# Performance work log

Hardware: AMD Instinct MI355X
Metric: run time of the kernel (lower is better)

The kernel has to match this reference:

```python
import jax, jax.numpy as jnp
import numpy as np

B, S, H, E, V = 64, 256, 1024, 256, 32000

def setup_inputs() -> dict:
    key = jax.random.key(0)
    ks = jax.random.split(key, 16)
    sc = 0.02
    return {
        'x': jax.random.randint(ks[0], (B, 1), 0, V),
        'dec_hs': jax.random.normal(ks[1], (1, B, H), jnp.float32),
        'enc_output': jax.random.normal(ks[2], (S, B, H), jnp.float32),
        'emb_table': jax.random.normal(ks[3], (V, E), jnp.float32) * sc,
        'w1_W': jax.random.normal(ks[4], (H, H), jnp.float32) * sc,
        'w1_b': jnp.zeros((H,), jnp.float32),
        'w2_W': jax.random.normal(ks[5], (H, H), jnp.float32) * sc,
        'w2_b': jnp.zeros((H,), jnp.float32),
        'v_W': jax.random.normal(ks[6], (1, H), jnp.float32) * sc,
        'v_b': jnp.zeros((1,), jnp.float32),
        'gru_W_ih': jax.random.normal(ks[7], (3 * H, H + E), jnp.float32) * sc,
        'gru_W_hh': jax.random.normal(ks[8], (3 * H, H), jnp.float32) * sc,
        'gru_b_ih': jnp.zeros((3 * H,), jnp.float32),
        'gru_b_hh': jnp.zeros((3 * H,), jnp.float32),
        'fc_W': jax.random.normal(ks[9], (V, H), jnp.float32) * sc,
        'fc_b': jnp.zeros((V,), jnp.float32),
    }

def reference(x, dec_hs, enc_output, emb_table, w1_W, w1_b, w2_W, w2_b,
              v_W, v_b, gru_W_ih, gru_W_hh, gru_b_ih, gru_b_hh, fc_W, fc_b):
    # ---- Bahdanau additive attention ----
    dec = jnp.transpose(dec_hs, (1, 0, 2))        # [B,1,H]
    enc = jnp.transpose(enc_output, (1, 0, 2))    # [B,S,H]
    feat = jnp.tanh(dec @ w1_W.T + w1_b + enc @ w2_W.T + w2_b)  # [B,S,H]
    scores = feat @ v_W.T + v_b                   # [B,S,1]
    attn = jax.nn.softmax(scores, axis=1)         # [B,S,1]
    context = jnp.sum(attn * enc, axis=1)         # [B,H]
    # ---- embedding lookup + concat ----
    emb = emb_table[x[:, 0]]                      # [B,E]
    gru_in = jnp.concatenate([context, emb], axis=-1)  # [B,H+E]
    # ---- single-step GRU (PyTorch gate convention) ----
    h = dec_hs[0]                                 # [B,H]
    gi = gru_in @ gru_W_ih.T + gru_b_ih           # [B,3H]
    gh = h @ gru_W_hh.T + gru_b_hh                # [B,3H]
    gi_r, gi_z, gi_n = jnp.split(gi, 3, axis=-1)
    gh_r, gh_z, gh_n = jnp.split(gh, 3, axis=-1)
    r = jax.nn.sigmoid(gi_r + gh_r)
    z = jax.nn.sigmoid(gi_z + gh_z)
    n = jnp.tanh(gi_n + r * gh_n)
    h_new = (1.0 - z) * n + z * h                 # [B,H]
    # ---- output projection ----
    fc_out = h_new @ fc_W.T + fc_b                # [B,V]
    return fc_out, h_new[None], attn
```

## Files before the change

### kernel.cpp

```cpp
#include <hip/hip_runtime.h>

#define BB 64
#define SS 256
#define HH 1024
#define EE 256
#define VV 32000

typedef unsigned short u16;
typedef __attribute__((ext_vector_type(4))) unsigned short u16x4;
typedef __attribute__((ext_vector_type(8))) short s16x8;
typedef __attribute__((ext_vector_type(4))) float f32x4;

typedef const void __attribute__((address_space(1)))* gas_p;
typedef void __attribute__((address_space(3)))* las_p;

__device__ __forceinline__ u16 f2bf(float f) {
  unsigned u = __builtin_bit_cast(unsigned, f);
  u += 0x7fffu + ((u >> 16) & 1u);
  return (u16)(u >> 16);
}
__device__ __forceinline__ float bf2f(u16 u) {
  return __builtin_bit_cast(float, ((unsigned)u) << 16);
}
__device__ __forceinline__ void gload16(const void* g, void* l) {
  __builtin_amdgcn_global_load_lds((gas_p)g, (las_p)l, 16, 0, 0);
}
#define MFMA16(a, b, c) __builtin_amdgcn_mfma_f32_16x16x32_bf16(a, b, c, 0, 0, 0)

__global__ __launch_bounds__(256) void k_convert(const float* __restrict__ enc,
    const float* __restrict__ w2, const float* __restrict__ dec,
    u16* __restrict__ Ap, u16* __restrict__ w2b, u16* __restrict__ hb) {
  int bid = blockIdx.x, t = threadIdx.x;
  const float* src;
  u16* dst;
  if (bid < BB * SS) {
    int b = bid >> 8, s = bid & 255;
    src = enc + (size_t)(s * BB + b) * HH;
    dst = Ap + (size_t)bid * HH;
  } else if (bid < BB * SS + HH) {
    int r = bid - BB * SS;
    src = w2 + (size_t)r * HH;
    dst = w2b + (size_t)r * HH;
  } else {
    int b = bid - (BB * SS + HH);
    src = dec + (size_t)b * HH;
    dst = hb + (size_t)b * HH;
  }
  f32x4 v = *(const f32x4*)(src + t * 4);
  u16x4 o = { f2bf(v[0]), f2bf(v[1]), f2bf(v[2]), f2bf(v[3]) };
  *(u16x4*)(dst + t * 4) = o;
}

__global__ __launch_bounds__(256) void k_dbmm(const u16* __restrict__ hb,
    const float* __restrict__ w1, float* __restrict__ dbp) {
  int kc = blockIdx.y;
  int kb = kc * 128;
  int n0 = blockIdx.x * 128;
  __shared__ u16 Ws[2][128 * 32];
  int t = threadIdx.x, lane = t & 63, w = t >> 6;
  int wm = w >> 1, wn = w & 1, l15 = lane & 15, lg = lane >> 4;
  f32x4 acc[2][4] = {};
  int kx = (lg ^ ((l15 >> 1) & 3)) * 8;
  int wrow = t >> 1, wh = t & 1;
  int xr = (wrow >> 1) & 3;
  int s0 = (2 * wh) ^ xr, s1 = (2 * wh + 1) ^ xr;
  const float* gW = w1 + (size_t)(n0 + wrow) * HH + kb + wh * 16;
  const u16* gA = hb + kb + lg * 8;
  f32x4 c0 = *(const f32x4*)(gW);
  f32x4 c1 = *(const f32x4*)(gW + 4);
  f32x4 c2 = *(const f32x4*)(gW + 8);
  f32x4 c3 = *(const f32x4*)(gW + 12);
  s16x8 a0 = *(const s16x8*)(gA + (size_t)(wm * 32 + l15) * HH);
  s16x8 a1 = *(const s16x8*)(gA + (size_t)(wm * 32 + 16 + l15) * HH);
  {
    u16* lw = &Ws[0][wrow * 32];
    u16x4 o0 = { f2bf(c0[0]), f2bf(c0[1]), f2bf(c0[2]), f2bf(c0[3]) };
    u16x4 o1 = { f2bf(c1[0]), f2bf(c1[1]), f2bf(c1[2]), f2bf(c1[3]) };
    u16x4 o2 = { f2bf(c2[0]), f2bf(c2[1]), f2bf(c2[2]), f2bf(c2[3]) };
    u16x4 o3 = { f2bf(c3[0]), f2bf(c3[1]), f2bf(c3[2]), f2bf(c3[3]) };
    *(u16x4*)(lw + s0 * 8) = o0; *(u16x4*)(lw + s0 * 8 + 4) = o1;
    *(u16x4*)(lw + s1 * 8) = o2; *(u16x4*)(lw + s1 * 8 + 4) = o3;
  }
  __syncthreads();
  for (int it = 0; it < 4; ++it) {
    int nlast = (it < 3);
    f32x4 n0v, n1v, n2v, n3v;
    s16x8 an0, an1;
    if (nlast) {
      int k1 = (it + 1) * 32;
      n0v = *(const f32x4*)(gW + k1);
      n1v = *(const f32x4*)(gW + k1 + 4);
      n2v = *(const f32x4*)(gW + k1 + 8);
      n3v = *(const f32x4*)(gW + k1 + 12);
      an0 = *(const s16x8*)(gA + (size_t)(wm * 32 + l15) * HH + k1);
      an1 = *(const s16x8*)(gA + (size_t)(wm * 32 + 16 + l15) * HH + k1);
    }
    const u16* wb = Ws[it & 1];
    s16x8 bfr[4];
#pragma unroll
    for (int ni = 0; ni < 4; ++ni)
      bfr[ni] = *(const s16x8*)&wb[(wn * 64 + ni * 16 + l15) * 32 + kx];
#pragma unroll
    for (int ni = 0; ni < 4; ++ni) {
      acc[0][ni] = MFMA16(a0, bfr[ni], acc[0][ni]);
      acc[1][ni] = MFMA16(a1, bfr[ni], acc[1][ni]);
    }
    if (nlast) {
      u16* lw = &Ws[(it + 1) & 1][wrow * 32];
      u16x4 o0 = { f2bf(n0v[0]), f2bf(n0v[1]), f2bf(n0v[2]), f2bf(n0v[3]) };
      u16x4 o1 = { f2bf(n1v[0]), f2bf(n1v[1]), f2bf(n1v[2]), f2bf(n1v[3]) };
      u16x4 o2 = { f2bf(n2v[0]), f2bf(n2v[1]), f2bf(n2v[2]), f2bf(n2v[3]) };
      u16x4 o3 = { f2bf(n3v[0]), f2bf(n3v[1]), f2bf(n3v[2]), f2bf(n3v[3]) };
      *(u16x4*)(lw + s0 * 8) = o0; *(u16x4*)(lw + s0 * 8 + 4) = o1;
      *(u16x4*)(lw + s1 * 8) = o2; *(u16x4*)(lw + s1 * 8 + 4) = o3;
      a0 = an0; a1 = an1;
    }
    __syncthreads();
  }
  float* Pb = dbp + (size_t)kc * 64 * HH;
#pragma unroll
  for (int mi = 0; mi < 2; ++mi)
#pragma unroll
    for (int ni = 0; ni < 4; ++ni)
#pragma unroll
      for (int r = 0; r < 4; ++r) {
        int m = wm * 32 + mi * 16 + lg * 4 + r;
        int n = n0 + wn * 64 + ni * 16 + l15;
        Pb[(size_t)m * HH + n] = acc[mi][ni][r];
      }
}

__global__ __launch_bounds__(256) void k_biggemm(const u16* __restrict__ Ap,
    const u16* __restrict__ Bw, const float* __restrict__ w1b,
    const float* __restrict__ w2bias, const float* __restrict__ dbp,
    const float* __restrict__ vW, float* __restrict__ sp) {
  __shared__ u16 As[128 * 64];
  __shared__ u16 Bs[128 * 64];
  __shared__ float sc[2][128];
  int bid = blockIdx.x;
  int mt = ((bid >> 6) << 3) | (bid & 7);
  int nt = (bid >> 3) & 7;
  int t = threadIdx.x, lane = t & 63, w = t >> 6;
  int wm = w >> 1, wn = w & 1, l15 = lane & 15, lg = lane >> 4;
  int m0 = mt * 128, n0 = nt * 128;
  int b = m0 >> 8;
  f32x4 acc[4][4] = {};
  int srow = w * 32 + (lane >> 3);
  int cswz = ((lane & 7) ^ (lane >> 3)) * 8;
  const u16* gA = Ap + (size_t)(m0 + srow) * HH + cswz;
  const u16* gB = Bw + (size_t)(n0 + srow) * HH + cswz;
  u16* lA = As + w * 32 * 64;
  u16* lB = Bs + w * 32 * 64;
  for (int it = 0; it < 16; ++it) {
    int k0 = it * 64;
#pragma unroll
    for (int i = 0; i < 4; ++i)
      gload16(gA + (size_t)i * 8 * HH + k0, lA + i * 8 * 64);
#pragma unroll
    for (int i = 0; i < 4; ++i)
      gload16(gB + (size_t)i * 8 * HH + k0, lB + i * 8 * 64);
    __syncthreads();
#pragma unroll
    for (int kk = 0; kk < 2; ++kk) {
      s16x8 af[4], bfr[4];
#pragma unroll
      for (int mi = 0; mi < 4; ++mi) {
        int row = wm * 64 + mi * 16 + l15;
        int slot = (kk * 4 + lg) ^ (row & 7);
        af[mi] = *(const s16x8*)&As[row * 64 + slot * 8];
      }
#pragma unroll
      for (int ni = 0; ni < 4; ++ni) {
        int row = wn * 64 + ni * 16 + l15;
        int slot = (kk * 4 + lg) ^ (row & 7);
        bfr[ni] = *(const s16x8*)&Bs[row * 64 + slot * 8];
      }
#pragma unroll
      for (int mi = 0; mi < 4; ++mi)
#pragma unroll
        for (int ni = 0; ni < 4; ++ni)
          acc[mi][ni] = MFMA16(af[mi], bfr[ni], acc[mi][ni]);
    }
    __syncthreads();
  }
  const float* vv = vW + n0;
  float dbs[4];
#pragma unroll
  for (int ni = 0; ni < 4; ++ni) {
    int nl = wn * 64 + ni * 16 + l15;
    int n = n0 + nl;
    float s = w1b[n] + w2bias[n];
#pragma unroll
    for (int p = 0; p < 8; ++p) s += dbp[(size_t)p * 64 * HH + (size_t)b * HH + n];
    dbs[ni] = s;
  }
#pragma unroll
  for (int mi = 0; mi < 4; ++mi) {
#pragma unroll
    for (int r = 0; r < 4; ++r) {
      float p = 0.f;
#pragma unroll
      for (int ni = 0; ni < 4; ++ni) {
        int nl = wn * 64 + ni * 16 + l15;
        p += tanhf(acc[mi][ni][r] + dbs[ni]) * vv[nl];
      }
      p += __shfl_xor(p, 1); p += __shfl_xor(p, 2);
      p += __shfl_xor(p, 4); p += __shfl_xor(p, 8);
      if (l15 == 0) sc[wn][wm * 64 + mi * 16 + lg * 4 + r] = p;
    }
  }
  __syncthreads();
  if (t < 128) sp[(size_t)(m0 + t) * 8 + nt] = sc[0][t] + sc[1][t];
}

__global__ __launch_bounds__(256) void k_ctxsm(const float* __restrict__ sp,
    const float* __restrict__ vb, const u16* __restrict__ Ap,
    float* __restrict__ attn, float* __restrict__ ctxp) {
  int sc = blockIdx.x, b = blockIdx.y, t = threadIdx.x;
  int lane = t & 63, w = t >> 6;
  const float* row = sp + (size_t)(b * SS + t) * 8;
  f32x4 a = *(const f32x4*)row;
  f32x4 c = *(const f32x4*)(row + 4);
  float score = a[0] + a[1] + a[2] + a[3] + c[0] + c[1] + c[2] + c[3] + vb[0];
  __shared__ float rmax[4], rsum[4], at[SS];
  float m = score;
  for (int mk = 1; mk < 64; mk <<= 1) m = fmaxf(m, __shfl_xor(m, mk));
  if (lane == 0) rmax[w] = m;
  __syncthreads();
  m = fmaxf(fmaxf(rmax[0], rmax[1]), fmaxf(rmax[2], rmax[3]));
  float e = expf(score - m);
  float ssum = e;
  for (int mk = 1; mk < 64; mk <<= 1) ssum += __shfl_xor(ssum, mk);
  if (lane == 0) rsum[w] = ssum;
  __syncthreads();
  float tot = rsum[0] + rsum[1] + rsum[2] + rsum[3];
  float av = e / tot;
  at[t] = av;
  if (sc == 0) attn[(size_t)b * SS + t] = av;
  __syncthreads();
  const u16* base = Ap + (size_t)(b * SS + sc * 32) * HH + t * 4;
  float a0 = 0.f, a1 = 0.f, a2 = 0.f, a3 = 0.f;
#pragma unroll 4
  for (int s = 0; s < 32; ++s) {
    u16x4 v = *(const u16x4*)(base + (size_t)s * HH);
    float w_ = at[sc * 32 + s];
    a0 += w_ * bf2f(v[0]); a1 += w_ * bf2f(v[1]);
    a2 += w_ * bf2f(v[2]); a3 += w_ * bf2f(v[3]);
  }
  f32x4 o = { a0, a1, a2, a3 };
  *(f32x4*)&ctxp[(size_t)(b * 8 + sc) * HH + t * 4] = o;
}

__global__ __launch_bounds__(256) void k_ctxcomb(const float* __restrict__ ctxp,
    const int* __restrict__ x, const float* __restrict__ emb,
    u16* __restrict__ gin) {
  int b = blockIdx.x, t = threadIdx.x;
  f32x4 s = {0.f, 0.f, 0.f, 0.f};
#pragma unroll
  for (int p = 0; p < 8; ++p)
    s += *(const f32x4*)&ctxp[(size_t)(b * 8 + p) * HH + t * 4];
  u16x4 o = { f2bf(s[0]), f2bf(s[1]), f2bf(s[2]), f2bf(s[3]) };
  *(u16x4*)(gin + (size_t)b * 1280 + t * 4) = o;
  int xb = x[b];
  gin[(size_t)b * 1280 + HH + t] = f2bf(emb[(size_t)xb * EE + t]);
}

__global__ __launch_bounds__(256) void k_gru(const u16* __restrict__ gin,
    const u16* __restrict__ hb, const float* __restrict__ Wih,
    const float* __restrict__ Whh, float* __restrict__ P) {
  int y = blockIdx.y;
  int z = (y >= 5);
  const u16* Ab = z ? hb : gin;
  const float* Wf = z ? Whh : Wih;
  int K = z ? HH : (HH + EE);
  int kb = (z ? (y - 5) : y) * 256;
  int n0 = blockIdx.x * 128;
  __shared__ u16 Ws[2][128 * 32];
  int t = threadIdx.x, lane = t & 63, w = t >> 6;
  int wm = w >> 1, wn = w & 1, l15 = lane & 15, lg = lane >> 4;
  f32x4 acc[2][4] = {};
  int kx = (lg ^ ((l15 >> 1) & 3)) * 8;
  int wrow = t >> 1, wh = t & 1;
  int xr = (wrow >> 1) & 3;
  int s0 = (2 * wh) ^ xr, s1 = (2 * wh + 1) ^ xr;
  const float* gW = Wf + (size_t)(n0 + wrow) * K + kb + wh * 16;
  const u16* gA = Ab + kb + lg * 8;
  f32x4 c0 = *(const f32x4*)(gW);
  f32x4 c1 = *(const f32x4*)(gW + 4);
  f32x4 c2 = *(const f32x4*)(gW + 8);
  f32x4 c3 = *(const f32x4*)(gW + 12);
  s16x8 a0 = *(const s16x8*)(gA + (size_t)(wm * 32 + l15) * K);
  s16x8 a1 = *(const s16x8*)(gA + (size_t)(wm * 32 + 16 + l15) * K);
  {
    u16* lw = &Ws[0][wrow * 32];
    u16x4 o0 = { f2bf(c0[0]), f2bf(c0[1]), f2bf(c0[2]), f2bf(c0[3]) };
    u16x4 o1 = { f2bf(c1[0]), f2bf(c1[1]), f2bf(c1[2]), f2bf(c1[3]) };
    u16x4 o2 = { f2bf(c2[0]), f2bf(c2[1]), f2bf(c2[2]), f2bf(c2[3]) };
    u16x4 o3 = { f2bf(c3[0]), f2bf(c3[1]), f2bf(c3[2]), f2bf(c3[3]) };
    *(u16x4*)(lw + s0 * 8) = o0; *(u16x4*)(lw + s0 * 8 + 4) = o1;
    *(u16x4*)(lw + s1 * 8) = o2; *(u16x4*)(lw + s1 * 8 + 4) = o3;
  }
  __syncthreads();
  for (int it = 0; it < 8; ++it) {
    int nlast = (it < 7);
    f32x4 n0v, n1v, n2v, n3v;
    s16x8 an0, an1;
    if (nlast) {
      int k1 = (it + 1) * 32;
      n0v = *(const f32x4*)(gW + k1);
      n1v = *(const f32x4*)(gW + k1 + 4);
      n2v = *(const f32x4*)(gW + k1 + 8);
      n3v = *(const f32x4*)(gW + k1 + 12);
      an0 = *(const s16x8*)(gA + (size_t)(wm * 32 + l15) * K + k1);
      an1 = *(const s16x8*)(gA + (size_t)(wm * 32 + 16 + l15) * K + k1);
    }
    const u16* wb = Ws[it & 1];
    s16x8 bfr[4];
#pragma unroll
    for (int ni = 0; ni < 4; ++ni)
      bfr[ni] = *(const s16x8*)&wb[(wn * 64 + ni * 16 + l15) * 32 + kx];
#pragma unroll
    for (int ni = 0; ni < 4; ++ni) {
      acc[0][ni] = MFMA16(a0, bfr[ni], acc[0][ni]);
      acc[1][ni] = MFMA16(a1, bfr[ni], acc[1][ni]);
    }
    if (nlast) {
      u16* lw = &Ws[(it + 1) & 1][wrow * 32];
      u16x4 o0 = { f2bf(n0v[0]), f2bf(n0v[1]), f2bf(n0v[2]), f2bf(n0v[3]) };
      u16x4 o1 = { f2bf(n1v[0]), f2bf(n1v[1]), f2bf(n1v[2]), f2bf(n1v[3]) };
      u16x4 o2 = { f2bf(n2v[0]), f2bf(n2v[1]), f2bf(n2v[2]), f2bf(n2v[3]) };
      u16x4 o3 = { f2bf(n3v[0]), f2bf(n3v[1]), f2bf(n3v[2]), f2bf(n3v[3]) };
      *(u16x4*)(lw + s0 * 8) = o0; *(u16x4*)(lw + s0 * 8 + 4) = o1;
      *(u16x4*)(lw + s1 * 8) = o2; *(u16x4*)(lw + s1 * 8 + 4) = o3;
      a0 = an0; a1 = an1;
    }
    __syncthreads();
  }
  float* Pb = P + (size_t)y * 64 * 3072;
#pragma unroll
  for (int mi = 0; mi < 2; ++mi)
#pragma unroll
    for (int ni = 0; ni < 4; ++ni)
#pragma unroll
      for (int r = 0; r < 4; ++r) {
        int m = wm * 32 + mi * 16 + lg * 4 + r;
        int n = n0 + wn * 64 + ni * 16 + l15;
        Pb[(size_t)m * 3072 + n] = acc[mi][ni][r];
      }
}

__global__ __launch_bounds__(256) void k_gates(const float* __restrict__ P,
    const float* __restrict__ bih, const float* __restrict__ bhh,
    const float* __restrict__ dec, float* __restrict__ hn_out,
    u16* __restrict__ hnb) {
  int b = blockIdx.x, t = threadIdx.x;
#pragma unroll
  for (int j = 0; j < 4; ++j) {
    int h = t + j * 256;
    float gir = 0.f, giz = 0.f, gin_ = 0.f, ghr = 0.f, ghz = 0.f, ghn = 0.f;
#pragma unroll
    for (int y = 0; y < 5; ++y) {
      const float* r = P + (size_t)(y * 64 + b) * 3072;
      gir += r[h]; giz += r[h + 1024]; gin_ += r[h + 2048];
    }
#pragma unroll
    for (int y = 0; y < 4; ++y) {
      const float* r = P + (size_t)((5 + y) * 64 + b) * 3072;
      ghr += r[h]; ghz += r[h + 1024]; ghn += r[h + 2048];
    }
    float rr = 1.f / (1.f + expf(-(gir + bih[h] + ghr + bhh[h])));
    float zz = 1.f / (1.f + expf(-(giz + bih[1024 + h] + ghz + bhh[1024 + h])));
    float nn = tanhf(gin_ + bih[2048 + h] + rr * (ghn + bhh[2048 + h]));
    float hv = dec[(size_t)b * HH + h];
    float hnew = (1.f - zz) * nn + zz * hv;
    hn_out[(size_t)b * HH + h] = hnew;
    hnb[(size_t)b * HH + h] = f2bf(hnew);
  }
}

__global__ __launch_bounds__(256) void k_fc(const u16* __restrict__ hnb,
    const float* __restrict__ W, const float* __restrict__ bias,
    float* __restrict__ out) {
  int n0 = blockIdx.x * 64;
  __shared__ u16 Ws[2][64 * 32];
  int t = threadIdx.x, lane = t & 63, w = t >> 6;
  int wm = w >> 1, wn = w & 1, l15 = lane & 15, lg = lane >> 4;
  f32x4 acc[2][2] = {};
  int kx = (lg ^ ((l15 >> 1) & 3)) * 8;
  int wrow = t >> 2;
  int sq = ((t & 3) ^ ((t >> 3) & 3)) * 8;
  const float* gW = W + (size_t)(n0 + wrow) * HH + (t & 3) * 8;
  const u16* gA = hnb + lg * 8;
  f32x4 c0 = *(const f32x4*)(gW);
  f32x4 c1 = *(const f32x4*)(gW + 4);
  s16x8 a0 = *(const s16x8*)(gA + (size_t)(wm * 32 + l15) * HH);
  s16x8 a1 = *(const s16x8*)(gA + (size_t)(wm * 32 + 16 + l15) * HH);
  {
    u16* lw = &Ws[0][wrow * 32 + sq];
    u16x4 o0 = { f2bf(c0[0]), f2bf(c0[1]), f2bf(c0[2]), f2bf(c0[3]) };
    u16x4 o1 = { f2bf(c1[0]), f2bf(c1[1]), f2bf(c1[2]), f2bf(c1[3]) };
    *(u16x4*)(lw) = o0; *(u16x4*)(lw + 4) = o1;
  }
  __syncthreads();
  for (int it = 0; it < 32; ++it) {
    int nlast = (it < 31);
    f32x4 n0v, n1v;
    s16x8 an0, an1;
    if (nlast) {
      int k1 = (it + 1) * 32;
      n0v = *(const f32x4*)(gW + k1);
      n1v = *(const f32x4*)(gW + k1 + 4);
      an0 = *(const s16x8*)(gA + (size_t)(wm * 32 + l15) * HH + k1);
      an1 = *(const s16x8*)(gA + (size_t)(wm * 32 + 16 + l15) * HH + k1);
    }
    const u16* wb = Ws[it & 1];
    s16x8 bfr[2];
#pragma unroll
    for (int ni = 0; ni < 2; ++ni)
      bfr[ni] = *(const s16x8*)&wb[(wn * 32 + ni * 16 + l15) * 32 + kx];
#pragma unroll
    for (int ni = 0; ni < 2; ++ni) {
      acc[0][ni] = MFMA16(a0, bfr[ni], acc[0][ni]);
      acc[1][ni] = MFMA16(a1, bfr[ni], acc[1][ni]);
    }
    if (nlast) {
      u16* lw = &Ws[(it + 1) & 1][wrow * 32 + sq];
      u16x4 o0 = { f2bf(n0v[0]), f2bf(n0v[1]), f2bf(n0v[2]), f2bf(n0v[3]) };
      u16x4 o1 = { f2bf(n1v[0]), f2bf(n1v[1]), f2bf(n1v[2]), f2bf(n1v[3]) };
      *(u16x4*)(lw) = o0; *(u16x4*)(lw + 4) = o1;
      a0 = an0; a1 = an1;
    }
    __syncthreads();
  }
#pragma unroll
  for (int mi = 0; mi < 2; ++mi)
#pragma unroll
    for (int ni = 0; ni < 2; ++ni)
#pragma unroll
      for (int r = 0; r < 4; ++r) {
        int m = wm * 32 + mi * 16 + lg * 4 + r;
        int n = n0 + wn * 32 + ni * 16 + l15;
        out[(size_t)m * VV + n] = acc[mi][ni][r] + bias[n];
      }
}

extern "C" void kernel_launch(void* const* d_in, const int* in_sizes, int n_in,
                              void* d_out, int out_size, void* d_ws, size_t ws_size,
                              hipStream_t stream) {
  const int*   x      = (const int*)   d_in[0];
  const float* dec    = (const float*) d_in[1];
  const float* enc    = (const float*) d_in[2];
  const float* emb    = (const float*) d_in[3];
  const float* w1     = (const float*) d_in[4];
  const float* w1b    = (const float*) d_in[5];
  const float* w2     = (const float*) d_in[6];
  const float* w2bias = (const float*) d_in[7];
  const float* vW     = (const float*) d_in[8];
  const float* vb     = (const float*) d_in[9];
  const float* Wih    = (const float*) d_in[10];
  const float* Whh    = (const float*) d_in[11];
  const float* bih    = (const float*) d_in[12];
  const float* bhh    = (const float*) d_in[13];
  const float* fcW    = (const float*) d_in[14];
  const float* fcb    = (const float*) d_in[15];
  float* out = (float*)d_out;
  char* ws = (char*)d_ws;
  u16*   Ap    = (u16*)(ws);
  u16*   w2b   = (u16*)(ws + 33554432);
  u16*   hb    = (u16*)(ws + 35651584);
  u16*   gin   = (u16*)(ws + 35782656);
  u16*   hnb   = (u16*)(ws + 35946496);
  float* sp    = (float*)(ws + 36339712);
  float* P     = (float*)(ws + 36864000);
  float* dbp   = P;
  float* ctxp  = P + 524288;
  float* hn   = out + 2048000;
  float* attn = out + 2113536;

  k_convert<<<BB * SS + HH + BB, 256, 0, stream>>>(enc, w2, dec, Ap, w2b, hb);
  k_dbmm<<<dim3(8, 8), 256, 0, stream>>>(hb, w1, dbp);
  k_biggemm<<<1024, 256, 0, stream>>>(Ap, w2b, w1b, w2bias, dbp, vW, sp);
  k_ctxsm<<<dim3(8, BB), 256, 0, stream>>>(sp, vb, Ap, attn, ctxp);
  k_ctxcomb<<<BB, 256, 0, stream>>>(ctxp, x, emb, gin);
  k_gru<<<dim3(24, 9), 256, 0, stream>>>(gin, hb, Wih, Whh, P);
  k_gates<<<BB, 256, 0, stream>>>(P, bih, bhh, dec, hn, hnb);
  k_fc<<<500, 256, 0, stream>>>(hnb, fcW, fcb, out);
}
```

Before: 145.9 us.

## Fuse convert with decoder matmul, switch big GEMM to 32x32 MFMA, widen gates grid

Merges the fp32-to-bf16 conversion kernel and the decoder-state projection into one launch: extra blocks compute the projection by converting dec directly instead of reading the bf16 copy. The attention GEMM uses 32x32x16 MFMA tiles instead of 16x16x32, which needs fewer LDS fragment loads per MFMA, and the epilogue reduction is adjusted to match. The gate kernel spreads each batch row over four blocks for more parallelism. Together these cut one launch and reduce LDS traffic, at the cost of more register pressure in the GEMM accumulators.

```diff
diff --git a/kernel.cpp b/kernel.cpp
--- a/kernel.cpp
+++ b/kernel.cpp
@@ -10,6 +10,7 @@
 typedef __attribute__((ext_vector_type(4))) unsigned short u16x4;
 typedef __attribute__((ext_vector_type(8))) short s16x8;
 typedef __attribute__((ext_vector_type(4))) float f32x4;
+typedef __attribute__((ext_vector_type(16))) float f32x16;
 
 typedef const void __attribute__((address_space(1)))* gas_p;
 typedef void __attribute__((address_space(3)))* las_p;
@@ -22,42 +23,54 @@
 __device__ __forceinline__ float bf2f(u16 u) {
   return __builtin_bit_cast(float, ((unsigned)u) << 16);
 }
+__device__ __forceinline__ s16x8 cvt8(f32x4 a, f32x4 b) {
+  s16x8 r;
+  r[0] = (short)f2bf(a[0]); r[1] = (short)f2bf(a[1]);
+  r[2] = (short)f2bf(a[2]); r[3] = (short)f2bf(a[3]);
+  r[4] = (short)f2bf(b[0]); r[5] = (short)f2bf(b[1]);
+  r[6] = (short)f2bf(b[2]); r[7] = (short)f2bf(b[3]);
+  return r;
+}
 __device__ __forceinline__ void gload16(const void* g, void* l) {
   __builtin_amdgcn_global_load_lds((gas_p)g, (las_p)l, 16, 0, 0);
 }
 #define MFMA16(a, b, c) __builtin_amdgcn_mfma_f32_16x16x32_bf16(a, b, c, 0, 0, 0)
-
-__global__ __launch_bounds__(256) void k_convert(const float* __restrict__ enc,
+#define MFMA32(a, b, c) __builtin_amdgcn_mfma_f32_32x32x16_bf16(a, b, c, 0, 0, 0)
+
+#define NCONV (BB * SS + HH + BB)
+__global__ __launch_bounds__(256) void k_convdb(const float* __restrict__ enc,
     const float* __restrict__ w2, const float* __restrict__ dec,
-    u16* __restrict__ Ap, u16* __restrict__ w2b, u16* __restrict__ hb) {
+    const float* __restrict__ w1,
+    u16* __restrict__ Ap, u16* __restrict__ w2b, u16* __restrict__ hb,
+    float* __restrict__ dbp) {
+  __shared__ u16 Ws[2][128 * 32];
   int bid = blockIdx.x, t = threadIdx.x;
-  const float* src;
-  u16* dst;
-  if (bid < BB * SS) {
-    int b = bid >> 8, s = bid & 255;
-    src = enc + (size_t)(s * BB + b) * HH;
-    dst = Ap + (size_t)bid * HH;
-  } else if (bid < BB * SS + HH) {
-    int r = bid - BB * SS;
-    src = w2 + (size_t)r * HH;
-    dst = w2b + (size_t)r * HH;
-  } else {
-    int b = bid - (BB * SS + HH);
-    src = dec + (size_t)b * HH;
-    dst = hb + (size_t)b * HH;
-  }
-  f32x4 v = *(const f32x4*)(src + t * 4);
-  u16x4 o = { f2bf(v[0]), f2bf(v[1]), f2bf(v[2]), f2bf(v[3]) };
-  *(u16x4*)(dst + t * 4) = o;
-}
-
-__global__ __launch_bounds__(256) void k_dbmm(const u16* __restrict__ hb,
-    const float* __restrict__ w1, float* __restrict__ dbp) {
-  int kc = blockIdx.y;
+  if (bid < NCONV) {
+    const float* src;
+    u16* dst;
+    if (bid < BB * SS) {
+      int b = bid >> 8, s = bid & 255;
+      src = enc + (size_t)(s * BB + b) * HH;
+      dst = Ap + (size_t)bid * HH;
+    } else if (bid < BB * SS + HH) {
+      int r = bid - BB * SS;
+      src = w2 + (size_t)r * HH;
+      dst = w2b + (size_t)r * HH;
+    } else {
+      int b = bid - (BB * SS + HH);
+      src = dec + (size_t)b * HH;
+      dst = hb + (size_t)b * HH;
+    }
+    f32x4 v = *(const f32x4*)(src + t * 4);
+    u16x4 o = { f2bf(v[0]), f2bf(v[1]), f2bf(v[2]), f2bf(v[3]) };
+    *(u16x4*)(dst + t * 4) = o;
+    return;
+  }
+  int bid2 = bid - NCONV;
+  int nt = bid2 & 7, kc = bid2 >> 3;
   int kb = kc * 128;
-  int n0 = blockIdx.x * 128;
-  __shared__ u16 Ws[2][128 * 32];
-  int t = threadIdx.x, lane = t & 63, w = t >> 6;
+  int n0 = nt * 128;
+  int lane = t & 63, w = t >> 6;
   int wm = w >> 1, wn = w & 1, l15 = lane & 15, lg = lane >> 4;
   f32x4 acc[2][4] = {};
   int kx = (lg ^ ((l15 >> 1) & 3)) * 8;
@@ -65,13 +78,15 @@
   int xr = (wrow >> 1) & 3;
   int s0 = (2 * wh) ^ xr, s1 = (2 * wh + 1) ^ xr;
   const float* gW = w1 + (size_t)(n0 + wrow) * HH + kb + wh * 16;
-  const u16* gA = hb + kb + lg * 8;
+  const float* dA = dec + kb + lg * 8;
   f32x4 c0 = *(const f32x4*)(gW);
   f32x4 c1 = *(const f32x4*)(gW + 4);
   f32x4 c2 = *(const f32x4*)(gW + 8);
   f32x4 c3 = *(const f32x4*)(gW + 12);
-  s16x8 a0 = *(const s16x8*)(gA + (size_t)(wm * 32 + l15) * HH);
-  s16x8 a1 = *(const s16x8*)(gA + (size_t)(wm * 32 + 16 + l15) * HH);
+  const float* r0 = dA + (size_t)(wm * 32 + l15) * HH;
+  const float* r1 = dA + (size_t)(wm * 32 + 16 + l15) * HH;
+  s16x8 a0 = cvt8(*(const f32x4*)r0, *(const f32x4*)(r0 + 4));
+  s16x8 a1 = cvt8(*(const f32x4*)r1, *(const f32x4*)(r1 + 4));
   {
     u16* lw = &Ws[0][wrow * 32];
     u16x4 o0 = { f2bf(c0[0]), f2bf(c0[1]), f2bf(c0[2]), f2bf(c0[3]) };
@@ -92,8 +107,8 @@
       n1v = *(const f32x4*)(gW + k1 + 4);
       n2v = *(const f32x4*)(gW + k1 + 8);
       n3v = *(const f32x4*)(gW + k1 + 12);
-      an0 = *(const s16x8*)(gA + (size_t)(wm * 32 + l15) * HH + k1);
-      an1 = *(const s16x8*)(gA + (size_t)(wm * 32 + 16 + l15) * HH + k1);
+      an0 = cvt8(*(const f32x4*)(r0 + k1), *(const f32x4*)(r0 + k1 + 4));
+      an1 = cvt8(*(const f32x4*)(r1 + k1), *(const f32x4*)(r1 + k1 + 4));
     }
     const u16* wb = Ws[it & 1];
     s16x8 bfr[4];
@@ -141,10 +156,11 @@
   int mt = ((bid >> 6) << 3) | (bid & 7);
   int nt = (bid >> 3) & 7;
   int t = threadIdx.x, lane = t & 63, w = t >> 6;
-  int wm = w >> 1, wn = w & 1, l15 = lane & 15, lg = lane >> 4;
+  int wm = w >> 1, wn = w & 1;
+  int l31 = lane & 31, lh = lane >> 5;
   int m0 = mt * 128, n0 = nt * 128;
   int b = m0 >> 8;
-  f32x4 acc[4][4] = {};
+  f32x16 acc[2][2] = {};
   int srow = w * 32 + (lane >> 3);
   int cswz = ((lane & 7) ^ (lane >> 3)) * 8;
   const u16* gA = Ap + (size_t)(m0 + srow) * HH + cswz;
@@ -161,52 +177,50 @@
       gload16(gB + (size_t)i * 8 * HH + k0, lB + i * 8 * 64);
     __syncthreads();
 #pragma unroll
-    for (int kk = 0; kk < 2; ++kk) {
-      s16x8 af[4], bfr[4];
-#pragma unroll
-      for (int mi = 0; mi < 4; ++mi) {
-        int row = wm * 64 + mi * 16 + l15;
-        int slot = (kk * 4 + lg) ^ (row & 7);
+    for (int kc = 0; kc < 4; ++kc) {
+      s16x8 af[2], bfr[2];
+#pragma unroll
+      for (int mi = 0; mi < 2; ++mi) {
+        int row = wm * 64 + mi * 32 + l31;
+        int slot = (kc * 2 + lh) ^ (row & 7);
         af[mi] = *(const s16x8*)&As[row * 64 + slot * 8];
       }
 #pragma unroll
-      for (int ni = 0; ni < 4; ++ni) {
-        int row = wn * 64 + ni * 16 + l15;
-        int slot = (kk * 4 + lg) ^ (row & 7);
+      for (int ni = 0; ni < 2; ++ni) {
+        int row = wn * 64 + ni * 32 + l31;
+        int slot = (kc * 2 + lh) ^ (row & 7);
         bfr[ni] = *(const s16x8*)&Bs[row * 64 + slot * 8];
       }
 #pragma unroll
-      for (int mi = 0; mi < 4; ++mi)
-#pragma unroll
-        for (int ni = 0; ni < 4; ++ni)
-          acc[mi][ni] = MFMA16(af[mi], bfr[ni], acc[mi][ni]);
+      for (int mi = 0; mi < 2; ++mi)
+#pragma unroll
+        for (int ni = 0; ni < 2; ++ni)
+          acc[mi][ni] = MFMA32(af[mi], bfr[ni], acc[mi][ni]);
     }
     __syncthreads();
   }
-  const float* vv = vW + n0;
-  float dbs[4];
-#pragma unroll
-  for (int ni = 0; ni < 4; ++ni) {
-    int nl = wn * 64 + ni * 16 + l15;
-    int n = n0 + nl;
+  float dbs[2], vvv[2];
+#pragma unroll
+  for (int ni = 0; ni < 2; ++ni) {
+    int n = n0 + wn * 64 + ni * 32 + l31;
     float s = w1b[n] + w2bias[n];
 #pragma unroll
-    for (int p = 0; p < 8; ++p) s += dbp[(size_t)p * 64 * HH + (size_t)b * HH + n];
+    for (int p = 0; p < 8; ++p)
+      s += dbp[(size_t)p * 64 * HH + (size_t)b * HH + n];
     dbs[ni] = s;
-  }
-#pragma unroll
-  for (int mi = 0; mi < 4; ++mi) {
-#pragma unroll
-    for (int r = 0; r < 4; ++r) {
-      float p = 0.f;
-#pragma unroll
-      for (int ni = 0; ni < 4; ++ni) {
-        int nl = wn * 64 + ni * 16 + l15;
-        p += tanhf(acc[mi][ni][r] + dbs[ni]) * vv[nl];
-      }
+    vvv[ni] = vW[n];
+  }
+#pragma unroll
+  for (int mi = 0; mi < 2; ++mi) {
+#pragma unroll
+    for (int r = 0; r < 16; ++r) {
+      float p = tanhf(acc[mi][0][r] + dbs[0]) * vvv[0]
+              + tanhf(acc[mi][1][r] + dbs[1]) * vvv[1];
       p += __shfl_xor(p, 1); p += __shfl_xor(p, 2);
       p += __shfl_xor(p, 4); p += __shfl_xor(p, 8);
-      if (l15 == 0) sc[wn][wm * 64 + mi * 16 + lg * 4 + r] = p;
+      p += __shfl_xor(p, 16);
+      if (l31 == 0)
+        sc[wn][wm * 64 + mi * 32 + (r & 3) + 8 * (r >> 2) + 4 * lh] = p;
     }
   }
   __syncthreads();
@@ -353,29 +367,26 @@
     const float* __restrict__ bih, const float* __restrict__ bhh,
     const float* __restrict__ dec, float* __restrict__ hn_out,
     u16* __restrict__ hnb) {
-  int b = blockIdx.x, t = threadIdx.x;
-#pragma unroll
-  for (int j = 0; j < 4; ++j) {
-    int h = t + j * 256;
-    float gir = 0.f, giz = 0.f, gin_ = 0.f, ghr = 0.f, ghz = 0.f, ghn = 0.f;
-#pragma unroll
-    for (int y = 0; y < 5; ++y) {
-      const float* r = P + (size_t)(y * 64 + b) * 3072;
-      gir += r[h]; giz += r[h + 1024]; gin_ += r[h + 2048];
-    }
-#pragma unroll
-    for (int y = 0; y < 4; ++y) {
-      const float* r = P + (size_t)((5 + y) * 64 + b) * 3072;
-      ghr += r[h]; ghz += r[h + 1024]; ghn += r[h + 2048];
-    }
-    float rr = 1.f / (1.f + expf(-(gir + bih[h] + ghr + bhh[h])));
-    float zz = 1.f / (1.f + expf(-(giz + bih[1024 + h] + ghz + bhh[1024 + h])));
-    float nn = tanhf(gin_ + bih[2048 + h] + rr * (ghn + bhh[2048 + h]));
-    float hv = dec[(size_t)b * HH + h];
-    float hnew = (1.f - zz) * nn + zz * hv;
-    hn_out[(size_t)b * HH + h] = hnew;
-    hnb[(size_t)b * HH + h] = f2bf(hnew);
-  }
+  int b = blockIdx.y, t = threadIdx.x;
+  int h = blockIdx.x * 256 + t;
+  float gir = 0.f, giz = 0.f, gin_ = 0.f, ghr = 0.f, ghz = 0.f, ghn = 0.f;
+#pragma unroll
+  for (int y = 0; y < 5; ++y) {
+    const float* r = P + (size_t)(y * 64 + b) * 3072;
+    gir += r[h]; giz += r[h + 1024]; gin_ += r[h + 2048];
+  }
+#pragma unroll
+  for (int y = 0; y < 4; ++y) {
+    const float* r = P + (size_t)((5 + y) * 64 + b) * 3072;
+    ghr += r[h]; ghz += r[h + 1024]; ghn += r[h + 2048];
+  }
+  float rr = 1.f / (1.f + expf(-(gir + bih[h] + ghr + bhh[h])));
+  float zz = 1.f / (1.f + expf(-(giz + bih[1024 + h] + ghz + bhh[1024 + h])));
+  float nn = tanhf(gin_ + bih[2048 + h] + rr * (ghn + bhh[2048 + h]));
+  float hv = dec[(size_t)b * HH + h];
+  float hnew = (1.f - zz) * nn + zz * hv;
+  hn_out[(size_t)b * HH + h] = hnew;
+  hnb[(size_t)b * HH + h] = f2bf(hnew);
 }
 
 __global__ __launch_bounds__(256) void k_fc(const u16* __restrict__ hnb,
@@ -477,12 +488,11 @@
   float* hn   = out + 2048000;
   float* attn = out + 2113536;
 
-  k_convert<<<BB * SS + HH + BB, 256, 0, stream>>>(enc, w2, dec, Ap, w2b, hb);
-  k_dbmm<<<dim3(8, 8), 256, 0, stream>>>(hb, w1, dbp);
+  k_convdb<<<NCONV + 64, 256, 0, stream>>>(enc, w2, dec, w1, Ap, w2b, hb, dbp);
   k_biggemm<<<1024, 256, 0, stream>>>(Ap, w2b, w1b, w2bias, dbp, vW, sp);
   k_ctxsm<<<dim3(8, BB), 256, 0, stream>>>(sp, vb, Ap, attn, ctxp);
   k_ctxcomb<<<BB, 256, 0, stream>>>(ctxp, x, emb, gin);
   k_gru<<<dim3(24, 9), 256, 0, stream>>>(gin, hb, Wih, Whh, P);
-  k_gates<<<BB, 256, 0, stream>>>(P, bih, bhh, dec, hn, hnb);
+  k_gates<<<dim3(4, BB), 256, 0, stream>>>(P, bih, bhh, dec, hn, hnb);
   k_fc<<<500, 256, 0, stream>>>(hnb, fcW, fcb, out);
 }
```

New measurement: 155.5 us. +6.6%, slower.

## Fuse dec-projection GEMM into convert kernel, widen GRU k-tile, spread gates grid

Applied to the files above, without the earlier changes.

Folds the small dec@W1 GEMM into the conversion kernel as extra blocks. Those blocks read dec in fp32 and convert it in registers, so they no longer wait on the bf16 hb buffer, and one launch is removed. The GRU GEMM k-step grows from 32 to 64, with a wider LDS tile and 8-way XOR swizzle, halving the barrier-separated iterations. The gates kernel is split over a 4x64 grid instead of 64 blocks to raise parallelism. The cost is more LDS and registers per GRU block, and a mixed-role fused kernel.

```diff
diff --git a/kernel.cpp b/kernel.cpp
--- a/kernel.cpp
+++ b/kernel.cpp
@@ -22,42 +22,53 @@
 __device__ __forceinline__ float bf2f(u16 u) {
   return __builtin_bit_cast(float, ((unsigned)u) << 16);
 }
+__device__ __forceinline__ s16x8 cvt8(f32x4 a, f32x4 b) {
+  s16x8 r;
+  r[0] = (short)f2bf(a[0]); r[1] = (short)f2bf(a[1]);
+  r[2] = (short)f2bf(a[2]); r[3] = (short)f2bf(a[3]);
+  r[4] = (short)f2bf(b[0]); r[5] = (short)f2bf(b[1]);
+  r[6] = (short)f2bf(b[2]); r[7] = (short)f2bf(b[3]);
+  return r;
+}
 __device__ __forceinline__ void gload16(const void* g, void* l) {
   __builtin_amdgcn_global_load_lds((gas_p)g, (las_p)l, 16, 0, 0);
 }
 #define MFMA16(a, b, c) __builtin_amdgcn_mfma_f32_16x16x32_bf16(a, b, c, 0, 0, 0)
 
-__global__ __launch_bounds__(256) void k_convert(const float* __restrict__ enc,
+#define NCONV (BB * SS + HH + BB)
+__global__ __launch_bounds__(256) void k_convdb(const float* __restrict__ enc,
     const float* __restrict__ w2, const float* __restrict__ dec,
-    u16* __restrict__ Ap, u16* __restrict__ w2b, u16* __restrict__ hb) {
+    const float* __restrict__ w1,
+    u16* __restrict__ Ap, u16* __restrict__ w2b, u16* __restrict__ hb,
+    float* __restrict__ dbp) {
+  __shared__ u16 Ws[2][128 * 32];
   int bid = blockIdx.x, t = threadIdx.x;
-  const float* src;
-  u16* dst;
-  if (bid < BB * SS) {
-    int b = bid >> 8, s = bid & 255;
-    src = enc + (size_t)(s * BB + b) * HH;
-    dst = Ap + (size_t)bid * HH;
-  } else if (bid < BB * SS + HH) {
-    int r = bid - BB * SS;
-    src = w2 + (size_t)r * HH;
-    dst = w2b + (size_t)r * HH;
-  } else {
-    int b = bid - (BB * SS + HH);
-    src = dec + (size_t)b * HH;
-    dst = hb + (size_t)b * HH;
-  }
-  f32x4 v = *(const f32x4*)(src + t * 4);
-  u16x4 o = { f2bf(v[0]), f2bf(v[1]), f2bf(v[2]), f2bf(v[3]) };
-  *(u16x4*)(dst + t * 4) = o;
-}
-
-__global__ __launch_bounds__(256) void k_dbmm(const u16* __restrict__ hb,
-    const float* __restrict__ w1, float* __restrict__ dbp) {
-  int kc = blockIdx.y;
+  if (bid < NCONV) {
+    const float* src;
+    u16* dst;
+    if (bid < BB * SS) {
+      int b = bid >> 8, s = bid & 255;
+      src = enc + (size_t)(s * BB + b) * HH;
+      dst = Ap + (size_t)bid * HH;
+    } else if (bid < BB * SS + HH) {
+      int r = bid - BB * SS;
+      src = w2 + (size_t)r * HH;
+      dst = w2b + (size_t)r * HH;
+    } else {
+      int b = bid - (BB * SS + HH);
+      src = dec + (size_t)b * HH;
+      dst = hb + (size_t)b * HH;
+    }
+    f32x4 v = *(const f32x4*)(src + t * 4);
+    u16x4 o = { f2bf(v[0]), f2bf(v[1]), f2bf(v[2]), f2bf(v[3]) };
+    *(u16x4*)(dst + t * 4) = o;
+    return;
+  }
+  int bid2 = bid - NCONV;
+  int nt = bid2 & 7, kc = bid2 >> 3;
   int kb = kc * 128;
-  int n0 = blockIdx.x * 128;
-  __shared__ u16 Ws[2][128 * 32];
-  int t = threadIdx.x, lane = t & 63, w = t >> 6;
+  int n0 = nt * 128;
+  int lane = t & 63, w = t >> 6;
   int wm = w >> 1, wn = w & 1, l15 = lane & 15, lg = lane >> 4;
   f32x4 acc[2][4] = {};
   int kx = (lg ^ ((l15 >> 1) & 3)) * 8;
@@ -65,13 +76,15 @@
   int xr = (wrow >> 1) & 3;
   int s0 = (2 * wh) ^ xr, s1 = (2 * wh + 1) ^ xr;
   const float* gW = w1 + (size_t)(n0 + wrow) * HH + kb + wh * 16;
-  const u16* gA = hb + kb + lg * 8;
+  const float* dA = dec + kb + lg * 8;
   f32x4 c0 = *(const f32x4*)(gW);
   f32x4 c1 = *(const f32x4*)(gW + 4);
   f32x4 c2 = *(const f32x4*)(gW + 8);
   f32x4 c3 = *(const f32x4*)(gW + 12);
-  s16x8 a0 = *(const s16x8*)(gA + (size_t)(wm * 32 + l15) * HH);
-  s16x8 a1 = *(const s16x8*)(gA + (size_t)(wm * 32 + 16 + l15) * HH);
+  const float* r0 = dA + (size_t)(wm * 32 + l15) * HH;
+  const float* r1 = dA + (size_t)(wm * 32 + 16 + l15) * HH;
+  s16x8 a0 = cvt8(*(const f32x4*)r0, *(const f32x4*)(r0 + 4));
+  s16x8 a1 = cvt8(*(const f32x4*)r1, *(const f32x4*)(r1 + 4));
   {
     u16* lw = &Ws[0][wrow * 32];
     u16x4 o0 = { f2bf(c0[0]), f2bf(c0[1]), f2bf(c0[2]), f2bf(c0[3]) };
@@ -92,8 +105,8 @@
       n1v = *(const f32x4*)(gW + k1 + 4);
       n2v = *(const f32x4*)(gW + k1 + 8);
       n3v = *(const f32x4*)(gW + k1 + 12);
-      an0 = *(const s16x8*)(gA + (size_t)(wm * 32 + l15) * HH + k1);
-      an1 = *(const s16x8*)(gA + (size_t)(wm * 32 + 16 + l15) * HH + k1);
+      an0 = cvt8(*(const f32x4*)(r0 + k1), *(const f32x4*)(r0 + k1 + 4));
+      an1 = cvt8(*(const f32x4*)(r1 + k1), *(const f32x4*)(r1 + k1 + 4));
     }
     const u16* wb = Ws[it & 1];
     s16x8 bfr[4];
@@ -275,64 +288,83 @@
   int K = z ? HH : (HH + EE);
   int kb = (z ? (y - 5) : y) * 256;
   int n0 = blockIdx.x * 128;
-  __shared__ u16 Ws[2][128 * 32];
+  __shared__ u16 Ws[2][128 * 64];
   int t = threadIdx.x, lane = t & 63, w = t >> 6;
   int wm = w >> 1, wn = w & 1, l15 = lane & 15, lg = lane >> 4;
   f32x4 acc[2][4] = {};
-  int kx = (lg ^ ((l15 >> 1) & 3)) * 8;
   int wrow = t >> 1, wh = t & 1;
-  int xr = (wrow >> 1) & 3;
-  int s0 = (2 * wh) ^ xr, s1 = (2 * wh + 1) ^ xr;
-  const float* gW = Wf + (size_t)(n0 + wrow) * K + kb + wh * 16;
+  int s_[4];
+#pragma unroll
+  for (int j = 0; j < 4; ++j) s_[j] = ((4 * wh + j) ^ (wrow & 7)) * 8;
+  const float* gW = Wf + (size_t)(n0 + wrow) * K + kb + wh * 32;
   const u16* gA = Ab + kb + lg * 8;
-  f32x4 c0 = *(const f32x4*)(gW);
-  f32x4 c1 = *(const f32x4*)(gW + 4);
-  f32x4 c2 = *(const f32x4*)(gW + 8);
-  f32x4 c3 = *(const f32x4*)(gW + 12);
-  s16x8 a0 = *(const s16x8*)(gA + (size_t)(wm * 32 + l15) * K);
-  s16x8 a1 = *(const s16x8*)(gA + (size_t)(wm * 32 + 16 + l15) * K);
+  const u16* rA0 = gA + (size_t)(wm * 32 + l15) * K;
+  const u16* rA1 = gA + (size_t)(wm * 32 + 16 + l15) * K;
+  f32x4 c0, c1, c2, c3, c4, c5, c6, c7;
+  c0 = *(const f32x4*)(gW);      c1 = *(const f32x4*)(gW + 4);
+  c2 = *(const f32x4*)(gW + 8);  c3 = *(const f32x4*)(gW + 12);
+  c4 = *(const f32x4*)(gW + 16); c5 = *(const f32x4*)(gW + 20);
+  c6 = *(const f32x4*)(gW + 24); c7 = *(const f32x4*)(gW + 28);
+  s16x8 a00 = *(const s16x8*)(rA0);
+  s16x8 a01 = *(const s16x8*)(rA0 + 32);
+  s16x8 a10 = *(const s16x8*)(rA1);
+  s16x8 a11 = *(const s16x8*)(rA1 + 32);
   {
-    u16* lw = &Ws[0][wrow * 32];
-    u16x4 o0 = { f2bf(c0[0]), f2bf(c0[1]), f2bf(c0[2]), f2bf(c0[3]) };
-    u16x4 o1 = { f2bf(c1[0]), f2bf(c1[1]), f2bf(c1[2]), f2bf(c1[3]) };
-    u16x4 o2 = { f2bf(c2[0]), f2bf(c2[1]), f2bf(c2[2]), f2bf(c2[3]) };
-    u16x4 o3 = { f2bf(c3[0]), f2bf(c3[1]), f2bf(c3[2]), f2bf(c3[3]) };
-    *(u16x4*)(lw + s0 * 8) = o0; *(u16x4*)(lw + s0 * 8 + 4) = o1;
-    *(u16x4*)(lw + s1 * 8) = o2; *(u16x4*)(lw + s1 * 8 + 4) = o3;
-  }
-  __syncthreads();
-  for (int it = 0; it < 8; ++it) {
-    int nlast = (it < 7);
-    f32x4 n0v, n1v, n2v, n3v;
-    s16x8 an0, an1;
+    u16* lw = &Ws[0][wrow * 64];
+    *(u16x4*)(lw + s_[0]) = (u16x4){ f2bf(c0[0]), f2bf(c0[1]), f2bf(c0[2]), f2bf(c0[3]) };
+    *(u16x4*)(lw + s_[0] + 4) = (u16x4){ f2bf(c1[0]), f2bf(c1[1]), f2bf(c1[2]), f2bf(c1[3]) };
+    *(u16x4*)(lw + s_[1]) = (u16x4){ f2bf(c2[0]), f2bf(c2[1]), f2bf(c2[2]), f2bf(c2[3]) };
+    *(u16x4*)(lw + s_[1] + 4) = (u16x4){ f2bf(c3[0]), f2bf(c3[1]), f2bf(c3[2]), f2bf(c3[3]) };
+    *(u16x4*)(lw + s_[2]) = (u16x4){ f2bf(c4[0]), f2bf(c4[1]), f2bf(c4[2]), f2bf(c4[3]) };
+    *(u16x4*)(lw + s_[2] + 4) = (u16x4){ f2bf(c5[0]), f2bf(c5[1]), f2bf(c5[2]), f2bf(c5[3]) };
+    *(u16x4*)(lw + s_[3]) = (u16x4){ f2bf(c6[0]), f2bf(c6[1]), f2bf(c6[2]), f2bf(c6[3]) };
+    *(u16x4*)(lw + s_[3] + 4) = (u16x4){ f2bf(c7[0]), f2bf(c7[1]), f2bf(c7[2]), f2bf(c7[3]) };
+  }
+  __syncthreads();
+  for (int it = 0; it < 4; ++it) {
+    int nlast = (it < 3);
+    f32x4 n0v, n1v, n2v, n3v, n4v, n5v, n6v, n7v;
+    s16x8 b00, b01, b10, b11;
     if (nlast) {
-      int k1 = (it + 1) * 32;
-      n0v = *(const f32x4*)(gW + k1);
-      n1v = *(const f32x4*)(gW + k1 + 4);
-      n2v = *(const f32x4*)(gW + k1 + 8);
-      n3v = *(const f32x4*)(gW + k1 + 12);
-      an0 = *(const s16x8*)(gA + (size_t)(wm * 32 + l15) * K + k1);
-      an1 = *(const s16x8*)(gA + (size_t)(wm * 32 + 16 + l15) * K + k1);
+      int k1 = (it + 1) * 64;
+      n0v = *(const f32x4*)(gW + k1);      n1v = *(const f32x4*)(gW + k1 + 4);
+      n2v = *(const f32x4*)(gW + k1 + 8);  n3v = *(const f32x4*)(gW + k1 + 12);
+      n4v = *(const f32x4*)(gW + k1 + 16); n5v = *(const f32x4*)(gW + k1 + 20);
+      n6v = *(const f32x4*)(gW + k1 + 24); n7v = *(const f32x4*)(gW + k1 + 28);
+      b00 = *(const s16x8*)(rA0 + k1);
+      b01 = *(const s16x8*)(rA0 + k1 + 32);
+      b10 = *(const s16x8*)(rA1 + k1);
+      b11 = *(const s16x8*)(rA1 + k1 + 32);
     }
     const u16* wb = Ws[it & 1];
-    s16x8 bfr[4];
-#pragma unroll
-    for (int ni = 0; ni < 4; ++ni)
-      bfr[ni] = *(const s16x8*)&wb[(wn * 64 + ni * 16 + l15) * 32 + kx];
-#pragma unroll
-    for (int ni = 0; ni < 4; ++ni) {
-      acc[0][ni] = MFMA16(a0, bfr[ni], acc[0][ni]);
-      acc[1][ni] = MFMA16(a1, bfr[ni], acc[1][ni]);
+#pragma unroll
+    for (int kk = 0; kk < 2; ++kk) {
+      s16x8 bfr[4];
+#pragma unroll
+      for (int ni = 0; ni < 4; ++ni) {
+        int row = wn * 64 + ni * 16 + l15;
+        int slot = (kk * 4 + lg) ^ (row & 7);
+        bfr[ni] = *(const s16x8*)&wb[row * 64 + slot * 8];
+      }
+      s16x8 fa0 = kk ? a01 : a00;
+      s16x8 fa1 = kk ? a11 : a10;
+#pragma unroll
+      for (int ni = 0; ni < 4; ++ni) {
+        acc[0][ni] = MFMA16(fa0, bfr[ni], acc[0][ni]);
+        acc[1][ni] = MFMA16(fa1, bfr[ni], acc[1][ni]);
+      }
     }
     if (nlast) {
-      u16* lw = &Ws[(it + 1) & 1][wrow * 32];
-      u16x4 o0 = { f2bf(n0v[0]), f2bf(n0v[1]), f2bf(n0v[2]), f2bf(n0v[3]) };
-      u16x4 o1 = { f2bf(n1v[0]), f2bf(n1v[1]), f2bf(n1v[2]), f2bf(n1v[3]) };
-      u16x4 o2 = { f2bf(n2v[0]), f2bf(n2v[1]), f2bf(n2v[2]), f2bf(n2v[3]) };
-      u16x4 o3 = { f2bf(n3v[0]), f2bf(n3v[1]), f2bf(n3v[2]), f2bf(n3v[3]) };
-      *(u16x4*)(lw + s0 * 8) = o0; *(u16x4*)(lw + s0 * 8 + 4) = o1;
-      *(u16x4*)(lw + s1 * 8) = o2; *(u16x4*)(lw + s1 * 8 + 4) = o3;
-      a0 = an0; a1 = an1;
+      u16* lw = &Ws[(it + 1) & 1][wrow * 64];
+      *(u16x4*)(lw + s_[0]) = (u16x4){ f2bf(n0v[0]), f2bf(n0v[1]), f2bf(n0v[2]), f2bf(n0v[3]) };
+      *(u16x4*)(lw + s_[0] + 4) = (u16x4){ f2bf(n1v[0]), f2bf(n1v[1]), f2bf(n1v[2]), f2bf(n1v[3]) };
+      *(u16x4*)(lw + s_[1]) = (u16x4){ f2bf(n2v[0]), f2bf(n2v[1]), f2bf(n2v[2]), f2bf(n2v[3]) };
+      *(u16x4*)(lw + s_[1] + 4) = (u16x4){ f2bf(n3v[0]), f2bf(n3v[1]), f2bf(n3v[2]), f2bf(n3v[3]) };
+      *(u16x4*)(lw + s_[2]) = (u16x4){ f2bf(n4v[0]), f2bf(n4v[1]), f2bf(n4v[2]), f2bf(n4v[3]) };
+      *(u16x4*)(lw + s_[2] + 4) = (u16x4){ f2bf(n5v[0]), f2bf(n5v[1]), f2bf(n5v[2]), f2bf(n5v[3]) };
+      *(u16x4*)(lw + s_[3]) = (u16x4){ f2bf(n6v[0]), f2bf(n6v[1]), f2bf(n6v[2]), f2bf(n6v[3]) };
+      *(u16x4*)(lw + s_[3] + 4) = (u16x4){ f2bf(n7v[0]), f2bf(n7v[1]), f2bf(n7v[2]), f2bf(n7v[3]) };
+      a00 = b00; a01 = b01; a10 = b10; a11 = b11;
     }
     __syncthreads();
   }
@@ -353,29 +385,26 @@
     const float* __restrict__ bih, const float* __restrict__ bhh,
     const float* __restrict__ dec, float* __restrict__ hn_out,
     u16* __restrict__ hnb) {
-  int b = blockIdx.x, t = threadIdx.x;
-#pragma unroll
-  for (int j = 0; j < 4; ++j) {
-    int h = t + j * 256;
-    float gir = 0.f, giz = 0.f, gin_ = 0.f, ghr = 0.f, ghz = 0.f, ghn = 0.f;
-#pragma unroll
-    for (int y = 0; y < 5; ++y) {
-      const float* r = P + (size_t)(y * 64 + b) * 3072;
-      gir += r[h]; giz += r[h + 1024]; gin_ += r[h + 2048];
-    }
-#pragma unroll
-    for (int y = 0; y < 4; ++y) {
-      const float* r = P + (size_t)((5 + y) * 64 + b) * 3072;
-      ghr += r[h]; ghz += r[h + 1024]; ghn += r[h + 2048];
-    }
-    float rr = 1.f / (1.f + expf(-(gir + bih[h] + ghr + bhh[h])));
-    float zz = 1.f / (1.f + expf(-(giz + bih[1024 + h] + ghz + bhh[1024 + h])));
-    float nn = tanhf(gin_ + bih[2048 + h] + rr * (ghn + bhh[2048 + h]));
-    float hv = dec[(size_t)b * HH + h];
-    float hnew = (1.f - zz) * nn + zz * hv;
-    hn_out[(size_t)b * HH + h] = hnew;
-    hnb[(size_t)b * HH + h] = f2bf(hnew);
-  }
+  int b = blockIdx.y, t = threadIdx.x;
+  int h = blockIdx.x * 256 + t;
+  float gir = 0.f, giz = 0.f, gin_ = 0.f, ghr = 0.f, ghz = 0.f, ghn = 0.f;
+#pragma unroll
+  for (int y = 0; y < 5; ++y) {
+    const float* r = P + (size_t)(y * 64 + b) * 3072;
+    gir += r[h]; giz += r[h + 1024]; gin_ += r[h + 2048];
+  }
+#pragma unroll
+  for (int y = 0; y < 4; ++y) {
+    const float* r = P + (size_t)((5 + y) * 64 + b) * 3072;
+    ghr += r[h]; ghz += r[h + 1024]; ghn += r[h + 2048];
+  }
+  float rr = 1.f / (1.f + expf(-(gir + bih[h] + ghr + bhh[h])));
+  float zz = 1.f / (1.f + expf(-(giz + bih[1024 + h] + ghz + bhh[1024 + h])));
+  float nn = tanhf(gin_ + bih[2048 + h] + rr * (ghn + bhh[2048 + h]));
+  float hv = dec[(size_t)b * HH + h];
+  float hnew = (1.f - zz) * nn + zz * hv;
+  hn_out[(size_t)b * HH + h] = hnew;
+  hnb[(size_t)b * HH + h] = f2bf(hnew);
 }
 
 __global__ __launch_bounds__(256) void k_fc(const u16* __restrict__ hnb,
@@ -477,12 +506,11 @@
   float* hn   = out + 2048000;
   float* attn = out + 2113536;
 
-  k_convert<<<BB * SS + HH + BB, 256, 0, stream>>>(enc, w2, dec, Ap, w2b, hb);
-  k_dbmm<<<dim3(8, 8), 256, 0, stream>>>(hb, w1, dbp);
+  k_convdb<<<NCONV + 64, 256, 0, stream>>>(enc, w2, dec, w1, Ap, w2b, hb, dbp);
   k_biggemm<<<1024, 256, 0, stream>>>(Ap, w2b, w1b, w2bias, dbp, vW, sp);
   k_ctxsm<<<dim3(8, BB), 256, 0, stream>>>(sp, vb, Ap, attn, ctxp);
   k_ctxcomb<<<BB, 256, 0, stream>>>(ctxp, x, emb, gin);
   k_gru<<<dim3(24, 9), 256, 0, stream>>>(gin, hb, Wih, Whh, P);
-  k_gates<<<BB, 256, 0, stream>>>(P, bih, bhh, dec, hn, hnb);
+  k_gates<<<dim3(4, BB), 256, 0, stream>>>(P, bih, bhh, dec, hn, hnb);
   k_fc<<<500, 256, 0, stream>>>(hnb, fcW, fcb, out);
 }
```

After: 152.1 us. 1.04x slower.
